# Optimization experiments

Hardware: AMD Instinct MI355X
Metric: run time of the kernel (lower is better)

The kernel has to match this reference:

```python
import jax, jax.numpy as jnp
import numpy as np
from jax import lax

MAP = 64  # spatial map resolution, hard-coded in the module


def setup_inputs() -> dict:
    key = jax.random.key(0)
    ks = jax.random.split(key, 6)
    B, N = 8, 17
    # valid boxes [x0,y0,x1,y1] inside the 64x64 map
    mins = jax.random.uniform(ks[0], (B, N, 2), jnp.float32) * 40.0
    sizes = jax.random.uniform(ks[1], (B, N, 2), jnp.float32) * 20.0 + 4.0
    bboxes = jnp.concatenate([mins, mins + sizes], axis=-1)  # [B,N,4]
    conv1_w = jax.random.normal(ks[2], (64, 2, 5, 5), jnp.float32) * 0.1
    conv1_b = jnp.zeros((64,), jnp.float32)
    conv2_w = jax.random.normal(ks[3], (32, 64, 5, 5), jnp.float32) * 0.05
    conv2_b = jnp.zeros((32,), jnp.float32)
    fc_w = jax.random.normal(ks[4], (512, 32), jnp.float32) * 0.1
    fc_b = jnp.zeros((512,), jnp.float32)
    return dict(bboxes=bboxes, conv1_w=conv1_w, conv1_b=conv1_b,
                conv2_w=conv2_w, conv2_b=conv2_b, fc_w=fc_w, fc_b=fc_b)


def _build_sp_maps(bboxes):
    # bboxes: [B,N,4] -> pairwise 2-channel binary maps [P, 2, 64, 64]
    B, N, _ = bboxes.shape
    iu, ju = jnp.triu_indices(N, k=1)           # P0 = N*(N-1)/2 pairs
    box_i = bboxes[:, iu]                       # [B,P0,4]
    box_j = bboxes[:, ju]                       # [B,P0,4]
    boxes = jnp.stack([box_i, box_j], axis=2)   # [B,P0,2,4]
    boxes = boxes.reshape(-1, 2, 4)             # [P,2,4]
    ys = jnp.arange(MAP, dtype=jnp.float32)[:, None]   # [64,1]
    xs = jnp.arange(MAP, dtype=jnp.float32)[None, :]   # [1,64]
    x0 = boxes[..., 0][..., None, None]
    y0 = boxes[..., 1][..., None, None]
    x1 = boxes[..., 2][..., None, None]
    y1 = boxes[..., 3][..., None, None]
    inside = (xs >= x0) & (xs < x1) & (ys >= y0) & (ys < y1)
    sp = inside.astype(bboxes.dtype)            # [P,2,64,64]
    # slicing tensor (batch, i, j) per pair
    P0 = iu.shape[0]
    b_idx = jnp.repeat(jnp.arange(B), P0)
    slicing = jnp.stack([b_idx, jnp.tile(iu, B), jnp.tile(ju, B)], axis=1)
    return sp, slicing


def _conv(x, w, b):
    y = lax.conv_general_dilated(x, w, (1, 1), 'VALID',
                                 dimension_numbers=('NCHW', 'OIHW', 'NCHW'))
    return y + b[None, :, None, None]


def _maxpool2(x):
    return lax.reduce_window(x, -jnp.inf, lax.max, (1, 1, 2, 2), (1, 1, 2, 2), 'VALID')


def reference(bboxes, conv1_w, conv1_b, conv2_w, conv2_b, fc_w, fc_b):
    sp, slicing = _build_sp_maps(bboxes)        # [P,2,64,64]
    h = _maxpool2(_conv(sp, conv1_w, conv1_b))  # [P,64,30,30]
    h = _maxpool2(_conv(h, conv2_w, conv2_b))   # [P,32,13,13]
    h = jnp.mean(h, axis=(2, 3))                # AvgPool(13) -> [P,32]
    feat = jax.nn.relu(h @ fc_w.T + fc_b)       # [P,512]
    return feat, slicing
```

## Files before the change

kernel.cpp:

```cpp
#include <hip/hip_runtime.h>
#include <hip/hip_bf16.h>


#define NPAIRS 1088
#define FEAT_SZ (NPAIRS * 512)

typedef float f32x16 __attribute__((ext_vector_type(16)));
typedef int v8i __attribute__((ext_vector_type(8)));
typedef float floatx2 __attribute__((ext_vector_type(2)));

#define WS_V 0
#define WS_C2B 14400
#define WS_BFRAG 14528

#define H1_PLANE 7200
#define H1_BYTES 57600
#define SM_V 57600
#define SM_HM 72000
#define SM_PART 72128
#define SMEM_BYTES 74176

__device__ __forceinline__ unsigned short f2bf(float f) {
  __hip_bfloat16 h = __float2bfloat16(f);
  unsigned short u;
  __builtin_memcpy(&u, &h, 2);
  return u;
}
__device__ __forceinline__ float bflo(unsigned int u) { return __uint_as_float(u << 16); }

__device__ __forceinline__ void fp8x8_to_f32(uint2 u, float* f) {
  floatx2 t;
  t = __builtin_amdgcn_cvt_pk_f32_fp8((int)u.x, false); f[0] = t.x; f[1] = t.y;
  t = __builtin_amdgcn_cvt_pk_f32_fp8((int)u.x, true);  f[2] = t.x; f[3] = t.y;
  t = __builtin_amdgcn_cvt_pk_f32_fp8((int)u.y, false); f[4] = t.x; f[5] = t.y;
  t = __builtin_amdgcn_cvt_pk_f32_fp8((int)u.y, true);  f[6] = t.x; f[7] = t.y;
}

__device__ __forceinline__ void pair_ij(int k, int* pi, int* pj) {
  int i = 0, rem = k;
  while (rem >= 16 - i) { rem -= 16 - i; ++i; }
  *pi = i;
  *pj = i + 1 + rem;
}

__device__ __forceinline__ int stz(int z, int a, int b) {
  if (z >= a) {
    if (z >= b) return 0;
    if (z <= b - 5) return 5;
    return 5 + (b - z);
  }
  if (z >= a - 4) return a - z;
  return 0;
}

__global__ void prep_kernel(const float* __restrict__ w1, const float* __restrict__ b1,
                            const float* __restrict__ w2, float* __restrict__ out,
                            unsigned char* __restrict__ ws) {
  int tid = blockIdx.x * blockDim.x + threadIdx.x;

  if (tid < 12800) {
    int o = tid & 63;
    int q = tid >> 6;
    int sx = q % 10; q /= 10;
    int sy = q % 10;
    int c = q / 10;
    int ky0 = (sy <= 4) ? sy : 0;
    int ky1 = (sy == 0) ? 0 : ((sy <= 5) ? 5 : sy - 5);
    int kx0 = (sx <= 4) ? sx : 0;
    int kx1 = (sx == 0) ? 0 : ((sx <= 5) ? 5 : sx - 5);
    const float* w = w1 + (o * 2 + c) * 25;
    float v = 0.f;
    for (int ky = ky0; ky < ky1; ++ky)
      for (int kx = kx0; kx < kx1; ++kx) v += w[ky * 5 + kx];
    unsigned qv = __builtin_amdgcn_cvt_pk_fp8_f32(v, v, 0, false);
    ((unsigned char*)(ws + WS_V))[(c * 100 + sy * 10 + sx) * 72 + o] = (unsigned char)(qv & 0xFF);
  } else if (tid < 12832) {
    int oc = tid - 12800;
    float s = 0.f;
    for (int ic = 0; ic < 64; ++ic) {
      const float* wp = w2 + (oc * 64 + ic) * 25;
      float t = 0.f;
      for (int q2 = 0; q2 < 25; ++q2) t += wp[q2];
      s += b1[ic] * t;
    }
    ((float*)(ws + WS_C2B))[oc] = s;
  } else if (tid < 13920) {
    int p = tid - 12832;
    int b = p / 136, k = p % 136, i, j;
    pair_ij(k, &i, &j);
    out[FEAT_SZ + p * 3 + 0] = (float)b;
    out[FEAT_SZ + p * 3 + 1] = (float)i;
    out[FEAT_SZ + p * 3 + 2] = (float)j;
  } else if (tid < 15520) {
    int idx = tid - 13920;
    int tap = idx >> 6, lane = idx & 63;
    int n = lane & 31, h = lane >> 5;
    unsigned qd[8];
#pragma unroll
    for (int d = 0; d < 8; ++d) {
      float v0 = w2[(n * 64 + h * 32 + 4 * d + 0) * 25 + tap];
      float v1 = w2[(n * 64 + h * 32 + 4 * d + 1) * 25 + tap];
      float v2 = w2[(n * 64 + h * 32 + 4 * d + 2) * 25 + tap];
      float v3 = w2[(n * 64 + h * 32 + 4 * d + 3) * 25 + tap];
      unsigned q = 0;
      q = __builtin_amdgcn_cvt_pk_fp8_f32(v0, v1, q, false);
      q = __builtin_amdgcn_cvt_pk_fp8_f32(v2, v3, q, true);
      qd[d] = q;
    }
    uint4* Bp = (uint4*)(ws + WS_BFRAG);
    Bp[tap * 128 + lane * 2 + 0] = make_uint4(qd[0], qd[1], qd[2], qd[3]);
    Bp[tap * 128 + lane * 2 + 1] = make_uint4(qd[4], qd[5], qd[6], qd[7]);
  }
}

__global__ __launch_bounds__(512, 4) void main_kernel(
    const float* __restrict__ bboxes, const float* __restrict__ b2,
    const float* __restrict__ fcw, const float* __restrict__ fcb,
    const unsigned char* __restrict__ ws, float* __restrict__ out) {
  __shared__ __align__(16) unsigned char smem[SMEM_BYTES];
  const int tid = threadIdx.x;
  const int lane = tid & 63;
  const int wid = tid >> 6;
  const int p = blockIdx.x;

  {
    const uint4* Vsrc = (const uint4*)(ws + WS_V);
    uint4* Vdst = (uint4*)(smem + SM_V);
    for (int i = tid; i < 900; i += 512) Vdst[i] = Vsrc[i];
  }

  int b = p / 136, k = p % 136, bi, bj;
  pair_ij(k, &bi, &bj);
  const float* bbA = bboxes + (b * 17 + bi) * 4;
  const float* bbB = bboxes + (b * 17 + bj) * 4;
  int ax[2], ay[2], bx[2], by[2];
  {
    auto cl = [](float v) { int t = (int)ceilf(v); return t < 0 ? 0 : (t > 64 ? 64 : t); };
    ax[0] = cl(bbA[0]); ay[0] = cl(bbA[1]); bx[0] = cl(bbA[2]); by[0] = cl(bbA[3]);
    ax[1] = cl(bbB[0]); ay[1] = cl(bbB[1]); bx[1] = cl(bbB[2]); by[1] = cl(bbB[3]);
  }
  __syncthreads();

  {
    for (int pos = tid; pos < 900; pos += 512) {
      int py = pos / 30, px = pos - py * 30;
      int oy = py * 2, ox = px * 2;
      int sy[2][2], sx[2][2];
#pragma unroll
      for (int c = 0; c < 2; ++c) {
        sy[c][0] = stz(oy, ay[c], by[c]);
        sy[c][1] = stz(oy + 1, ay[c], by[c]);
        sx[c][0] = stz(ox, ax[c], bx[c]);
        sx[c][1] = stz(ox + 1, ax[c], bx[c]);
      }
      bool e0 = ((sy[0][0] | sy[0][1]) == 0) || ((sx[0][0] | sx[0][1]) == 0);
      bool e1 = ((sy[1][0] | sy[1][1]) == 0) || ((sx[1][0] | sx[1][1]) == 0);
      unsigned hbase = (unsigned)pos * 8u;
      if (e0 && e1) {
#pragma unroll
        for (int g = 0; g < 8; ++g)
          *(uint2*)(smem + hbase + g * H1_PLANE) = make_uint2(0u, 0u);
        continue;
      }

      unsigned r0o[4], r1o[4];
#pragma unroll
      for (int dy = 0; dy < 2; ++dy)
#pragma unroll
        for (int dx = 0; dx < 2; ++dx) {
          r0o[dy * 2 + dx] = SM_V + (unsigned)(sy[0][dy] * 10 + sx[0][dx]) * 72u;
          r1o[dy * 2 + dx] = SM_V + 7200u + (unsigned)(sy[1][dy] * 10 + sx[1][dx]) * 72u;
        }

#pragma unroll
      for (int g = 0; g < 8; ++g) {
        float mx[8];
#pragma unroll
        for (int sp = 0; sp < 4; ++sp) {
          uint2 u0 = *(const uint2*)(smem + r0o[sp] + g * 8);
          uint2 u1 = *(const uint2*)(smem + r1o[sp] + g * 8);
          float a[8], c[8];
          fp8x8_to_f32(u0, a);
          fp8x8_to_f32(u1, c);
#pragma unroll
          for (int d = 0; d < 8; ++d) {
            float v = a[d] + c[d];
            mx[d] = (sp == 0) ? v : fmaxf(mx[d], v);
          }
        }
        unsigned q0 = 0, q1 = 0;
        q0 = __builtin_amdgcn_cvt_pk_fp8_f32(mx[0], mx[1], q0, false);
        q0 = __builtin_amdgcn_cvt_pk_fp8_f32(mx[2], mx[3], q0, true);
        q1 = __builtin_amdgcn_cvt_pk_fp8_f32(mx[4], mx[5], q1, false);
        q1 = __builtin_amdgcn_cvt_pk_fp8_f32(mx[6], mx[7], q1, true);
        *(uint2*)(smem + hbase + g * H1_PLANE) = make_uint2(q0, q1);
      }
    }
  }
  __syncthreads();

  const int oc = lane & 31;
  const float c2bb = ((const float*)(ws + WS_C2B))[oc] + b2[oc];

  int s0a = ay[0] - 4 < 0 ? 0 : ay[0] - 4;
  int s0b = ay[1] - 4 < 0 ? 0 : ay[1] - 4;
  int pre0 = s0a < s0b ? s0a : s0b;
  int e0a = by[0] < 60 ? by[0] : 60;
  int e0b = by[1] < 60 ? by[1] : 60;
  int pre1 = e0a > e0b ? e0a : e0b;
  int pr0 = pre0 >> 1, pr1 = (pre1 - 1) >> 1;
  int or0 = pr0 - 4 < 0 ? 0 : pr0 - 4;
  int or1 = pr1 > 25 ? 25 : pr1;
  int poslo = or0 * 26, poshi = (or1 + 1) * 26;
  int t_first = poslo >> 5;
  int t_last = (poshi - 1) >> 5;

  int tb[3]; int acts[3]; unsigned vb[3]; bool anyact = false;
  const unsigned hvo = (unsigned)(lane >> 5) * (4u * H1_PLANE);
#pragma unroll
  for (int ti = 0; ti < 3; ++ti) {
    int t = t_first + wid + ti * 8;
    bool a = (t <= t_last);
    acts[ti] = __builtin_amdgcn_readfirstlane(a ? 1 : 0);
    anyact |= a;
    tb[ti] = t * 32;
    int pos = tb[ti] + (lane & 31);
    if (pos > 675) pos = 675;
    int oy2 = pos / 26, ox2 = pos - oy2 * 26;
    vb[ti] = (unsigned)(oy2 * 30 + ox2) * 8u + hvo;
  }

  f32x16 acc[3];
#pragma unroll
  for (int ti = 0; ti < 3; ++ti)
#pragma unroll
    for (int r = 0; r < 16; ++r) acc[ti][r] = 0.f;

  if (anyact) {
    const uint4* Bp = (const uint4*)(ws + WS_BFRAG);
    uint4 bc0 = Bp[lane * 2 + 0];
    uint4 bc1 = Bp[lane * 2 + 1];
#pragma unroll
    for (int t = 0; t < 25; ++t) {
      uint4 bn0, bn1;
      if (t < 24) {
        bn0 = Bp[(t + 1) * 128 + lane * 2 + 0];
        bn1 = Bp[(t + 1) * 128 + lane * 2 + 1];
      }
      const int dtap = ((t / 5) * 30 + (t % 5)) * 8;
      v8i bop = (v8i){(int)bc0.x, (int)bc0.y, (int)bc0.z, (int)bc0.w,
                      (int)bc1.x, (int)bc1.y, (int)bc1.z, (int)bc1.w};
#pragma unroll
      for (int ti = 0; ti < 3; ++ti) {
        if (!acts[ti]) continue;
        uint2 a0 = *(const uint2*)(smem + vb[ti] + 0 * H1_PLANE + dtap);
        uint2 a1 = *(const uint2*)(smem + vb[ti] + 1 * H1_PLANE + dtap);
        uint2 a2 = *(const uint2*)(smem + vb[ti] + 2 * H1_PLANE + dtap);
        uint2 a3 = *(const uint2*)(smem + vb[ti] + 3 * H1_PLANE + dtap);
        v8i aop = (v8i){(int)a0.x, (int)a0.y, (int)a1.x, (int)a1.y,
                        (int)a2.x, (int)a2.y, (int)a3.x, (int)a3.y};
        acc[ti] = __builtin_amdgcn_mfma_scale_f32_32x32x64_f8f6f4(
            aop, bop, acc[ti], 0, 0, 0, 0x7F7F7F7F, 0, 0x7F7F7F7F);
      }
      bc0 = bn0; bc1 = bn1;
    }
  }
  __syncthreads();

  unsigned short* c2 = (unsigned short*)smem;
#pragma unroll
  for (int ti = 0; ti < 3; ++ti) {
    if (!acts[ti]) continue;
#pragma unroll
    for (int r = 0; r < 16; ++r) {
      int row = (r & 3) + 8 * (r >> 2) + 4 * (lane >> 5);
      int pos = tb[ti] + row;
      if (pos < 676) c2[pos * 36 + oc] = f2bf(acc[ti][r] + c2bb);
    }
  }
  {
    unsigned short cu = f2bf(c2bb);
#pragma unroll
    for (int ti = 0; ti < 3; ++ti) {
      int tf = wid + ti * 8;
      if (tf < 22 && (tf < t_first || tf > t_last)) {
#pragma unroll
        for (int r = 0; r < 16; ++r) {
          int row = (r & 3) + 8 * (r >> 2) + 4 * (lane >> 5);
          int pos = tf * 32 + row;
          if (pos < 676) c2[pos * 36 + oc] = cu;
        }
      }
    }
  }
  __syncthreads();

  {
    float* partial = (float*)(smem + SM_PART);
    int moc = lane & 31;
    int mi = wid * 2 + (lane >> 5);
    float ssum = 0.f;
    for (int q = mi; q < 169; q += 16) {
      int py = q / 13, px = q - py * 13;
      int p0 = (py * 2) * 26 + px * 2;
      float v00 = bflo(c2[p0 * 36 + moc]);
      float v01 = bflo(c2[(p0 + 1) * 36 + moc]);
      float v10 = bflo(c2[(p0 + 26) * 36 + moc]);
      float v11 = bflo(c2[(p0 + 27) * 36 + moc]);
      ssum += fmaxf(fmaxf(v00, v01), fmaxf(v10, v11));
    }
    partial[mi * 32 + moc] = ssum;
  }
  __syncthreads();
  if (tid < 32) {
    const float* partial = (const float*)(smem + SM_PART);
    float s = 0.f;
#pragma unroll
    for (int mi = 0; mi < 16; ++mi) s += partial[mi * 32 + tid];
    ((float*)(smem + SM_HM))[tid] = s * (1.0f / 169.0f);
  }
  __syncthreads();

  {
    const float* hm = (const float*)(smem + SM_HM);
    float a = fcb[tid];
    const float* wrow = fcw + tid * 32;
#pragma unroll 8
    for (int o2 = 0; o2 < 32; ++o2) a = fmaf(hm[o2], wrow[o2], a);
    out[p * 512 + tid] = fmaxf(a, 0.f);
  }
}

extern "C" void kernel_launch(void* const* d_in, const int* in_sizes, int n_in,
                              void* d_out, int out_size, void* d_ws, size_t ws_size,
                              hipStream_t stream) {
  const float* bboxes = (const float*)d_in[0];
  const float* w1 = (const float*)d_in[1];
  const float* b1 = (const float*)d_in[2];
  const float* w2 = (const float*)d_in[3];
  const float* b2 = (const float*)d_in[4];
  const float* fcw = (const float*)d_in[5];
  const float* fcb = (const float*)d_in[6];
  float* out = (float*)d_out;
  unsigned char* ws = (unsigned char*)d_ws;

  hipLaunchKernelGGL(prep_kernel, dim3(80), dim3(256), 0, stream, w1, b1, w2, out, ws);
  hipLaunchKernelGGL(main_kernel, dim3(NPAIRS), dim3(512), 0, stream, bboxes, b2, fcw, fcb, ws, out);
}
```

Baseline: 70.24 us.

## Skip unused conv1 rows, deepen B prefetch, pack bf16 conv2 stores, widen prep

Several changes land together. conv1 pooled-map rows outside the band that the active conv2 tiles read are now skipped. The conv2 weight-fragment prefetch becomes a 3-deep ring instead of single-step double buffering. The conv2 output is stored channel-major as packed bf16 pairs, so the 2x2 max-pool reads two words instead of four halves. The prep kernel spreads fp8 weight packing across more threads, and the FC loop uses float4 weight loads. The trade-offs are extra registers from the deeper prefetch and new layout indexing, which depends on pos-pair alignment.

```diff
diff --git a/kernel.cpp b/kernel.cpp
--- a/kernel.cpp
+++ b/kernel.cpp
@@ -27,6 +27,7 @@
   return u;
 }
 __device__ __forceinline__ float bflo(unsigned int u) { return __uint_as_float(u << 16); }
+__device__ __forceinline__ float bfhi(unsigned int u) { return __uint_as_float(u & 0xffff0000u); }
 
 __device__ __forceinline__ void fp8x8_to_f32(uint2 u, float* f) {
   floatx2 t;
@@ -91,25 +92,21 @@
     out[FEAT_SZ + p * 3 + 0] = (float)b;
     out[FEAT_SZ + p * 3 + 1] = (float)i;
     out[FEAT_SZ + p * 3 + 2] = (float)j;
-  } else if (tid < 15520) {
+  } else if (tid < 26720) {
     int idx = tid - 13920;
-    int tap = idx >> 6, lane = idx & 63;
+    int d = idx & 7;
+    int lane = (idx >> 3) & 63;
+    int tap = idx >> 9;
     int n = lane & 31, h = lane >> 5;
-    unsigned qd[8];
-#pragma unroll
-    for (int d = 0; d < 8; ++d) {
-      float v0 = w2[(n * 64 + h * 32 + 4 * d + 0) * 25 + tap];
-      float v1 = w2[(n * 64 + h * 32 + 4 * d + 1) * 25 + tap];
-      float v2 = w2[(n * 64 + h * 32 + 4 * d + 2) * 25 + tap];
-      float v3 = w2[(n * 64 + h * 32 + 4 * d + 3) * 25 + tap];
-      unsigned q = 0;
-      q = __builtin_amdgcn_cvt_pk_fp8_f32(v0, v1, q, false);
-      q = __builtin_amdgcn_cvt_pk_fp8_f32(v2, v3, q, true);
-      qd[d] = q;
-    }
-    uint4* Bp = (uint4*)(ws + WS_BFRAG);
-    Bp[tap * 128 + lane * 2 + 0] = make_uint4(qd[0], qd[1], qd[2], qd[3]);
-    Bp[tap * 128 + lane * 2 + 1] = make_uint4(qd[4], qd[5], qd[6], qd[7]);
+    int icb = h * 32 + d * 4;
+    float v0 = w2[(n * 64 + icb + 0) * 25 + tap];
+    float v1 = w2[(n * 64 + icb + 1) * 25 + tap];
+    float v2 = w2[(n * 64 + icb + 2) * 25 + tap];
+    float v3 = w2[(n * 64 + icb + 3) * 25 + tap];
+    unsigned q = 0;
+    q = __builtin_amdgcn_cvt_pk_fp8_f32(v0, v1, q, false);
+    q = __builtin_amdgcn_cvt_pk_fp8_f32(v2, v3, q, true);
+    ((unsigned*)(ws + WS_BFRAG))[tap * 512 + lane * 8 + d] = q;
   }
 }
 
@@ -139,68 +136,6 @@
     ax[0] = cl(bbA[0]); ay[0] = cl(bbA[1]); bx[0] = cl(bbA[2]); by[0] = cl(bbA[3]);
     ax[1] = cl(bbB[0]); ay[1] = cl(bbB[1]); bx[1] = cl(bbB[2]); by[1] = cl(bbB[3]);
   }
-  __syncthreads();
-
-  {
-    for (int pos = tid; pos < 900; pos += 512) {
-      int py = pos / 30, px = pos - py * 30;
-      int oy = py * 2, ox = px * 2;
-      int sy[2][2], sx[2][2];
-#pragma unroll
-      for (int c = 0; c < 2; ++c) {
-        sy[c][0] = stz(oy, ay[c], by[c]);
-        sy[c][1] = stz(oy + 1, ay[c], by[c]);
-        sx[c][0] = stz(ox, ax[c], bx[c]);
-        sx[c][1] = stz(ox + 1, ax[c], bx[c]);
-      }
-      bool e0 = ((sy[0][0] | sy[0][1]) == 0) || ((sx[0][0] | sx[0][1]) == 0);
-      bool e1 = ((sy[1][0] | sy[1][1]) == 0) || ((sx[1][0] | sx[1][1]) == 0);
-      unsigned hbase = (unsigned)pos * 8u;
-      if (e0 && e1) {
-#pragma unroll
-        for (int g = 0; g < 8; ++g)
-          *(uint2*)(smem + hbase + g * H1_PLANE) = make_uint2(0u, 0u);
-        continue;
-      }
-
-      unsigned r0o[4], r1o[4];
-#pragma unroll
-      for (int dy = 0; dy < 2; ++dy)
-#pragma unroll
-        for (int dx = 0; dx < 2; ++dx) {
-          r0o[dy * 2 + dx] = SM_V + (unsigned)(sy[0][dy] * 10 + sx[0][dx]) * 72u;
-          r1o[dy * 2 + dx] = SM_V + 7200u + (unsigned)(sy[1][dy] * 10 + sx[1][dx]) * 72u;
-        }
-
-#pragma unroll
-      for (int g = 0; g < 8; ++g) {
-        float mx[8];
-#pragma unroll
-        for (int sp = 0; sp < 4; ++sp) {
-          uint2 u0 = *(const uint2*)(smem + r0o[sp] + g * 8);
-          uint2 u1 = *(const uint2*)(smem + r1o[sp] + g * 8);
-          float a[8], c[8];
-          fp8x8_to_f32(u0, a);
-          fp8x8_to_f32(u1, c);
-#pragma unroll
-          for (int d = 0; d < 8; ++d) {
-            float v = a[d] + c[d];
-            mx[d] = (sp == 0) ? v : fmaxf(mx[d], v);
-          }
-        }
-        unsigned q0 = 0, q1 = 0;
-        q0 = __builtin_amdgcn_cvt_pk_fp8_f32(mx[0], mx[1], q0, false);
-        q0 = __builtin_amdgcn_cvt_pk_fp8_f32(mx[2], mx[3], q0, true);
-        q1 = __builtin_amdgcn_cvt_pk_fp8_f32(mx[4], mx[5], q1, false);
-        q1 = __builtin_amdgcn_cvt_pk_fp8_f32(mx[6], mx[7], q1, true);
-        *(uint2*)(smem + hbase + g * H1_PLANE) = make_uint2(q0, q1);
-      }
-    }
-  }
-  __syncthreads();
-
-  const int oc = lane & 31;
-  const float c2bb = ((const float*)(ws + WS_C2B))[oc] + b2[oc];
 
   int s0a = ay[0] - 4 < 0 ? 0 : ay[0] - 4;
   int s0b = ay[1] - 4 < 0 ? 0 : ay[1] - 4;
@@ -215,6 +150,74 @@
   int t_first = poslo >> 5;
   int t_last = (poshi - 1) >> 5;
 
+  int pos_end = (t_last + 1) * 32; if (pos_end > 676) pos_end = 676;
+  int zr0 = (t_first * 32) / 26;
+  int zr1 = (pos_end - 1) / 26 + 4; if (zr1 > 29) zr1 = 29;
+
+  __syncthreads();
+
+  {
+    for (int pos = tid; pos < 900; pos += 512) {
+      int py = pos / 30, px = pos - py * 30;
+      if (py < zr0 || py > zr1) continue;
+      int oy = py * 2, ox = px * 2;
+      int sy[2][2], sx[2][2];
+#pragma unroll
+      for (int c = 0; c < 2; ++c) {
+        sy[c][0] = stz(oy, ay[c], by[c]);
+        sy[c][1] = stz(oy + 1, ay[c], by[c]);
+        sx[c][0] = stz(ox, ax[c], bx[c]);
+        sx[c][1] = stz(ox + 1, ax[c], bx[c]);
+      }
+      bool e0 = ((sy[0][0] | sy[0][1]) == 0) || ((sx[0][0] | sx[0][1]) == 0);
+      bool e1 = ((sy[1][0] | sy[1][1]) == 0) || ((sx[1][0] | sx[1][1]) == 0);
+      unsigned hbase = (unsigned)pos * 8u;
+      if (e0 && e1) {
+#pragma unroll
+        for (int g = 0; g < 8; ++g)
+          *(uint2*)(smem + hbase + g * H1_PLANE) = make_uint2(0u, 0u);
+        continue;
+      }
+
+      unsigned r0o[4], r1o[4];
+#pragma unroll
+      for (int dy = 0; dy < 2; ++dy)
+#pragma unroll
+        for (int dx = 0; dx < 2; ++dx) {
+          r0o[dy * 2 + dx] = SM_V + (unsigned)(sy[0][dy] * 10 + sx[0][dx]) * 72u;
+          r1o[dy * 2 + dx] = SM_V + 7200u + (unsigned)(sy[1][dy] * 10 + sx[1][dx]) * 72u;
+        }
+
+#pragma unroll
+      for (int g = 0; g < 8; ++g) {
+        float mx[8];
+#pragma unroll
+        for (int sp = 0; sp < 4; ++sp) {
+          uint2 u0 = *(const uint2*)(smem + r0o[sp] + g * 8);
+          uint2 u1 = *(const uint2*)(smem + r1o[sp] + g * 8);
+          float a[8], c[8];
+          fp8x8_to_f32(u0, a);
+          fp8x8_to_f32(u1, c);
+#pragma unroll
+          for (int d = 0; d < 8; ++d) {
+            float v = a[d] + c[d];
+            mx[d] = (sp == 0) ? v : fmaxf(mx[d], v);
+          }
+        }
+        unsigned q0 = 0, q1 = 0;
+        q0 = __builtin_amdgcn_cvt_pk_fp8_f32(mx[0], mx[1], q0, false);
+        q0 = __builtin_amdgcn_cvt_pk_fp8_f32(mx[2], mx[3], q0, true);
+        q1 = __builtin_amdgcn_cvt_pk_fp8_f32(mx[4], mx[5], q1, false);
+        q1 = __builtin_amdgcn_cvt_pk_fp8_f32(mx[6], mx[7], q1, true);
+        *(uint2*)(smem + hbase + g * H1_PLANE) = make_uint2(q0, q1);
+      }
+    }
+  }
+  __syncthreads();
+
+  const int oc = lane & 31;
+  const float c2bb = ((const float*)(ws + WS_C2B))[oc] + b2[oc];
+
   int tb[3]; int acts[3]; unsigned vb[3]; bool anyact = false;
   const unsigned hvo = (unsigned)(lane >> 5) * (4u * H1_PLANE);
 #pragma unroll
@@ -238,14 +241,19 @@
 
   if (anyact) {
     const uint4* Bp = (const uint4*)(ws + WS_BFRAG);
-    uint4 bc0 = Bp[lane * 2 + 0];
-    uint4 bc1 = Bp[lane * 2 + 1];
+    uint4 b0[3], b1[3];
+#pragma unroll
+    for (int t = 0; t < 3; ++t) {
+      b0[t] = Bp[t * 128 + lane * 2 + 0];
+      b1[t] = Bp[t * 128 + lane * 2 + 1];
+    }
 #pragma unroll
     for (int t = 0; t < 25; ++t) {
-      uint4 bn0, bn1;
-      if (t < 24) {
-        bn0 = Bp[(t + 1) * 128 + lane * 2 + 0];
-        bn1 = Bp[(t + 1) * 128 + lane * 2 + 1];
+      const int sl = t % 3;
+      uint4 bc0 = b0[sl], bc1 = b1[sl];
+      if (t + 3 < 25) {
+        b0[sl] = Bp[(t + 3) * 128 + lane * 2 + 0];
+        b1[sl] = Bp[(t + 3) * 128 + lane * 2 + 1];
       }
       const int dtap = ((t / 5) * 30 + (t % 5)) * 8;
       v8i bop = (v8i){(int)bc0.x, (int)bc0.y, (int)bc0.z, (int)bc0.w,
@@ -262,33 +270,39 @@
         acc[ti] = __builtin_amdgcn_mfma_scale_f32_32x32x64_f8f6f4(
             aop, bop, acc[ti], 0, 0, 0, 0x7F7F7F7F, 0, 0x7F7F7F7F);
       }
-      bc0 = bn0; bc1 = bn1;
-    }
-  }
-  __syncthreads();
-
-  unsigned short* c2 = (unsigned short*)smem;
+    }
+  }
+  __syncthreads();
+
+  unsigned* c2w = (unsigned*)smem;
+  const int oc353 = oc * 353;
 #pragma unroll
   for (int ti = 0; ti < 3; ++ti) {
     if (!acts[ti]) continue;
 #pragma unroll
-    for (int r = 0; r < 16; ++r) {
+    for (int rp = 0; rp < 8; ++rp) {
+      int r = 2 * rp;
       int row = (r & 3) + 8 * (r >> 2) + 4 * (lane >> 5);
       int pos = tb[ti] + row;
-      if (pos < 676) c2[pos * 36 + oc] = f2bf(acc[ti][r] + c2bb);
+      float lo = acc[ti][r] + c2bb, hi = acc[ti][r + 1] + c2bb;
+      unsigned pk;
+      asm("v_cvt_pk_bf16_f32 %0, %1, %2" : "=v"(pk) : "v"(lo), "v"(hi));
+      c2w[oc353 + (pos >> 1)] = pk;
     }
   }
   {
     unsigned short cu = f2bf(c2bb);
+    unsigned cupk = (unsigned)cu | ((unsigned)cu << 16);
 #pragma unroll
     for (int ti = 0; ti < 3; ++ti) {
       int tf = wid + ti * 8;
       if (tf < 22 && (tf < t_first || tf > t_last)) {
 #pragma unroll
-        for (int r = 0; r < 16; ++r) {
+        for (int rp = 0; rp < 8; ++rp) {
+          int r = 2 * rp;
           int row = (r & 3) + 8 * (r >> 2) + 4 * (lane >> 5);
           int pos = tf * 32 + row;
-          if (pos < 676) c2[pos * 36 + oc] = cu;
+          c2w[oc353 + (pos >> 1)] = cupk;
         }
       }
     }
@@ -297,16 +311,18 @@
 
   {
     float* partial = (float*)(smem + SM_PART);
+    const unsigned* c2r = (const unsigned*)smem;
     int moc = lane & 31;
     int mi = wid * 2 + (lane >> 5);
+    int m353 = moc * 353;
     float ssum = 0.f;
     for (int q = mi; q < 169; q += 16) {
       int py = q / 13, px = q - py * 13;
-      int p0 = (py * 2) * 26 + px * 2;
-      float v00 = bflo(c2[p0 * 36 + moc]);
-      float v01 = bflo(c2[(p0 + 1) * 36 + moc]);
-      float v10 = bflo(c2[(p0 + 26) * 36 + moc]);
-      float v11 = bflo(c2[(p0 + 27) * 36 + moc]);
+      int halfp = py * 26 + px;
+      unsigned ua = c2r[m353 + halfp];
+      unsigned ub = c2r[m353 + halfp + 13];
+      float v00 = bflo(ua), v01 = bfhi(ua);
+      float v10 = bflo(ub), v11 = bfhi(ub);
       ssum += fmaxf(fmaxf(v00, v01), fmaxf(v10, v11));
     }
     partial[mi * 32 + moc] = ssum;
@@ -323,10 +339,16 @@
 
   {
     const float* hm = (const float*)(smem + SM_HM);
+    const float4* wrow4 = (const float4*)(fcw + tid * 32);
     float a = fcb[tid];
-    const float* wrow = fcw + tid * 32;
-#pragma unroll 8
-    for (int o2 = 0; o2 < 32; ++o2) a = fmaf(hm[o2], wrow[o2], a);
+#pragma unroll
+    for (int q = 0; q < 8; ++q) {
+      float4 w = wrow4[q];
+      a = fmaf(hm[4 * q + 0], w.x, a);
+      a = fmaf(hm[4 * q + 1], w.y, a);
+      a = fmaf(hm[4 * q + 2], w.z, a);
+      a = fmaf(hm[4 * q + 3], w.w, a);
+    }
     out[p * 512 + tid] = fmaxf(a, 0.f);
   }
 }
@@ -344,6 +366,6 @@
   float* out = (float*)d_out;
   unsigned char* ws = (unsigned char*)d_ws;
 
-  hipLaunchKernelGGL(prep_kernel, dim3(80), dim3(256), 0, stream, w1, b1, w2, out, ws);
+  hipLaunchKernelGGL(prep_kernel, dim3(105), dim3(256), 0, stream, w1, b1, w2, out, ws);
   hipLaunchKernelGGL(main_kernel, dim3(NPAIRS), dim3(512), 0, stream, bboxes, b2, fcw, fcb, ws, out);
 }
```

New measurement: 66.56 us. 1.06x faster.
